# Kernel tuning notes

Hardware: AMD Instinct MI355X
Metric: run time of the kernel (lower is better)

Reference implementation:

```python
import jax, jax.numpy as jnp
import numpy as np

NUM_AGENTS = 32
N_OBS = 16
K = 5
N = 2 * NUM_AGENTS + N_OBS          # 80 nodes per graph
E_KNN = N * K                        # knn edges (loop=True)
E = E_KNN + N_OBS                    # + agent->goal edges (arange(n_obstacles) quirk of source)
AGENT_R = 0.05
OBST_SIZES = np.full((N_OBS,), 0.1, dtype=np.float32)
HID = 128


def _build_graph(obstacle_pos, agent_pos, goal_pos, agent_vel):
    # pos: agents, goals, obstacles
    pos = jnp.concatenate([agent_pos, goal_pos, obstacle_pos], axis=0)        # [N,2]
    d2 = jnp.sum((pos[:, None, :] - pos[None, :, :]) ** 2, axis=-1)           # [N,N]
    _, nbr = jax.lax.top_k(-d2, K)                                            # [N,K] k-NN incl self
    knn_src = nbr.reshape(-1)
    knn_dst = jnp.repeat(jnp.arange(N), K)
    ag_src = jnp.arange(N_OBS)
    ag_dst = ag_src + NUM_AGENTS
    src = jnp.concatenate([knn_src, ag_src])                                  # [E]
    dst = jnp.concatenate([knn_dst, ag_dst])
    # torch.unique(edge_index, dim=-1) dedup: knn edges are unique by construction;
    # only appended agent->goal edges can duplicate -> mask them out.
    dup = ((ag_src * N + ag_dst)[:, None] == (knn_src * N + knn_dst)[None, :]).any(axis=-1)
    mask = jnp.concatenate([jnp.ones((E_KNN,), dtype=bool), ~dup])
    radius = jnp.zeros((N,)).at[:NUM_AGENTS].set(AGENT_R).at[2 * NUM_AGENTS:].set(jnp.asarray(OBST_SIZES))
    x = jnp.zeros((N, 5))
    x = x.at[:NUM_AGENTS, 0].set(1.0)
    x = x.at[NUM_AGENTS:2 * NUM_AGENTS, 1].set(1.0)
    x = x.at[2 * NUM_AGENTS:, 2].set(1.0)
    x = x.at[:NUM_AGENTS, 3].set(jnp.linalg.norm(agent_vel, axis=-1))
    x = x.at[:, 4].set(radius)
    pd = pos[src] - pos[dst]
    dist = jnp.linalg.norm(pd, axis=-1)
    vel = jnp.zeros((N, 2)).at[:NUM_AGENTS].set(agent_vel)
    rv = vel[src] - vel[dst]
    pdn = pd / jnp.maximum(dist, 1e-6)[:, None]
    flag = ((src < NUM_AGENTS) & (dst == src + NUM_AGENTS)).astype(pos.dtype)
    ea = jnp.stack([flag, dist, dist - (radius[src] + radius[dst]),
                    jnp.sum(rv * pdn, axis=-1),
                    rv[:, 0] * pdn[:, 1] - rv[:, 1] * pdn[:, 0]], axis=-1)     # [E,5]
    return x, src, dst, ea, mask


def _gatv2(x, src, dst, ea, mask, Wl, bl, Wr, br, We, att, bias):
    # GATv2Conv, heads=1, add_self_loops=False, edge_dim=5
    xl = x @ Wl + bl                                    # [N,F] (messages)
    xr = x @ Wr + br                                    # [N,F]
    e = jax.nn.leaky_relu(xl[src] + xr[dst] + ea @ We, 0.2)   # [E,F]
    logit = e @ att                                     # [E]
    logit = jnp.where(mask, logit, jnp.finfo(logit.dtype).min)
    m = jax.ops.segment_max(logit, dst, num_segments=N)
    a = jnp.where(mask, jnp.exp(logit - m[dst]), 0.0)
    denom = jax.ops.segment_sum(a, dst, num_segments=N)
    alpha = a / denom[dst]
    out = jax.ops.segment_sum(alpha[:, None] * xl[src], dst, num_segments=N)
    return out + bias


def _forward_single(obstacle_pos, agent_pos, goal_pos, agent_vel, params):
    x, src, dst, ea, mask = _build_graph(obstacle_pos, agent_pos, goal_pos, agent_vel)
    h = x
    for i, p in enumerate(params):
        h = _gatv2(h, src, dst, ea, mask, *p)
        if i < len(params) - 1:
            h = jax.nn.relu(h)
    # global_add_pool over agent nodes (agents are first NUM_AGENTS nodes)
    return jnp.sum(h[:NUM_AGENTS, 0])


def reference(obstacle_pos, agent_pos, goal_pos, agent_vel,
              Wl1, bl1, Wr1, br1, We1, att1, bias1,
              Wl2, bl2, Wr2, br2, We2, att2, bias2,
              Wl3, bl3, Wr3, br3, We3, att3, bias3):
    params = [(Wl1, bl1, Wr1, br1, We1, att1, bias1),
              (Wl2, bl2, Wr2, br2, We2, att2, bias2),
              (Wl3, bl3, Wr3, br3, We3, att3, bias3)]
    vals = jax.vmap(lambda o, a, g, v: _forward_single(o, a, g, v, params))(
        obstacle_pos, agent_pos, goal_pos, agent_vel)                       # [B]
    B = vals.shape[0]
    return jnp.broadcast_to(vals[:, None, None], (B, NUM_AGENTS, 1))


def setup_inputs() -> dict:
    key = jax.random.key(0)
    ks = jax.random.split(key, 32)
    B = 1024
    inp = {
        "obstacle_pos": jax.random.normal(ks[0], (B, N_OBS, 2), dtype=jnp.float32),
        "agent_pos": jax.random.normal(ks[1], (B, NUM_AGENTS, 2), dtype=jnp.float32),
        "goal_pos": jax.random.normal(ks[2], (B, NUM_AGENTS, 2), dtype=jnp.float32),
        "agent_vel": jax.random.normal(ks[3], (B, NUM_AGENTS, 2), dtype=jnp.float32) * 0.1,
    }
    dims = [(5, HID), (HID, HID), (HID, 1)]
    ki = 4
    for li, (fi, fo) in enumerate(dims, start=1):
        s = float(np.sqrt(2.0 / (fi + fo)))
        se = float(np.sqrt(2.0 / (5 + fo)))
        inp[f"Wl{li}"] = jax.random.normal(ks[ki], (fi, fo)) * s; ki += 1
        inp[f"bl{li}"] = jnp.zeros((fo,))
        inp[f"Wr{li}"] = jax.random.normal(ks[ki], (fi, fo)) * s; ki += 1
        inp[f"br{li}"] = jnp.zeros((fo,))
        inp[f"We{li}"] = jax.random.normal(ks[ki], (5, fo)) * se; ki += 1
        inp[f"att{li}"] = jax.random.normal(ks[ki], (fo,)) * float(1.0 / np.sqrt(fo)); ki += 1
        inp[f"bias{li}"] = jnp.zeros((fo,))
    return inp
```

## Files before the change

### kernel.cpp

```cpp
#include <hip/hip_runtime.h>
#include <math.h>

typedef float floatx4 __attribute__((ext_vector_type(4)));
typedef short bf16x8  __attribute__((ext_vector_type(8)));

#define NAG   32
#define NOBS  16
#define NN    80
#define KK    5
#define EKNN  400
#define ED    416
#define HID   128
#define TPB   1024

__device__ __forceinline__ int bsw(int n, int c) { return c ^ ((n & 7) << 1); }

__device__ __forceinline__ float bfhi_f(unsigned u) {
    union { unsigned u; float f; } v; v.u = u & 0xffff0000u; return v.f;
}
__device__ __forceinline__ float bflo_f(unsigned u) {
    union { unsigned u; float f; } v; v.u = u << 16; return v.f;
}
__device__ __forceinline__ unsigned f_bf_rne(float f) {
    union { float f; unsigned u; } v; v.f = f;
    return (v.u + 0x7fffu + ((v.u >> 16) & 1u)) >> 16;
}
__device__ __forceinline__ uint2 pack_bf4v(floatx4 a) {
    uint2 r;
    r.x = f_bf_rne(a[0]) | (f_bf_rne(a[1]) << 16);
    r.y = f_bf_rne(a[2]) | (f_bf_rne(a[3]) << 16);
    return r;
}
__device__ __forceinline__ floatx4 unpack_bf4v(uint2 p) {
    floatx4 r;
    r[0] = bflo_f(p.x); r[1] = bfhi_f(p.x);
    r[2] = bflo_f(p.y); r[3] = bfhi_f(p.y);
    return r;
}

__device__ __forceinline__ void nl_pass5(const float* xf,
    const float* __restrict__ W, const float* __restrict__ bv,
    uint2* dstB, int t)
{
    const int q  = t & 31;
    const int ng = t >> 5;
    const int n0 = ng, n1 = ng + 32, n2 = 64 + (ng & 15);
    floatx4 a0 = {0.f,0.f,0.f,0.f}, a1 = a0, a2 = a0;
#pragma unroll
    for (int fi = 0; fi < 5; ++fi) {
        floatx4 wv = *(const floatx4*)(W + fi*HID + q*4);
        a0 += xf[n0*5 + fi] * wv;
        a1 += xf[n1*5 + fi] * wv;
        a2 += xf[n2*5 + fi] * wv;
    }
    floatx4 b4 = *(const floatx4*)(bv + q*4);
    a0 += b4; a1 += b4; a2 += b4;
    dstB[n0*32 + bsw(n0, q)] = pack_bf4v(a0);
    dstB[n1*32 + bsw(n1, q)] = pack_bf4v(a1);
    if (ng < 16) dstB[n2*32 + bsw(n2, q)] = pack_bf4v(a2);
}

__device__ __forceinline__ void store_tile(floatx4 ac, int mtbase, int l, int col,
                                           float bval, char* dbase)
{
#pragma unroll
    for (int rr = 0; rr < 4; rr++) {
        int row = mtbase + ((l >> 4) << 2) + rr;
        int ch  = (col >> 2) ^ ((row & 7) << 1);
        *(unsigned short*)(dbase + row*256 + ch*8 + (col & 3)*2) =
            (unsigned short)f_bf_rne(ac[rr] + bval);
    }
}

__device__ __forceinline__ void edge_mfma(const uint2* xlB, const uint2* xrB,
    const uint4* WeBfT, const uint4* eaB, const unsigned short* sdS,
    const int* gmask, const float* attS, float* logitS, int t)
{
    const int w = t >> 6, l = t & 63;
    const int g = l >> 4, e16 = l & 15;
    const bf16x8 zf = {0,0,0,0,0,0,0,0};

#pragma unroll 1
    for (int rep = 0; rep < 2; rep++) {
        const int mt = w + rep*16;
        if (mt >= 26) break;
        const int e = mt*16 + e16;
        const unsigned sdv = sdS[e];
        const int src = sdv & 0xff, dst = sdv >> 8;
        const int sb = src*32, db = dst*32;
        const int sx = (src & 7) << 1, dx = (dst & 7) << 1;
        bf16x8 bfrag = (l < 16) ? ((const bf16x8*)eaB)[e] : zf;
        float partial = 0.f;

#pragma unroll 1
        for (int ct = 0; ct < 8; ct++) {
            bf16x8 afrag = (l < 16) ? ((const bf16x8*)WeBfT)[ct*16 + e16] : zf;
            floatx4 D = {0.f,0.f,0.f,0.f};
            D = __builtin_amdgcn_mfma_f32_16x16x32_bf16(afrag, bfrag, D, 0, 0, 0);
            floatx4 attv = ((const floatx4*)attS)[ct*4 + g];
            floatx4 xlv = unpack_bf4v(xlB[sb + ((4*ct + g) ^ sx)]);
            floatx4 xrv = unpack_bf4v(xrB[db + ((4*ct + g) ^ dx)]);
#pragma unroll
            for (int rr = 0; rr < 4; rr++) {
                float s = D[rr] + xlv[rr] + xrv[rr];
                float m = fmaxf(s, 0.2f*s);
                partial = fmaf(m, attv[rr], partial);
            }
        }
        partial += __shfl_xor(partial, 16);
        partial += __shfl_xor(partial, 32);
        if (l < 16) {
            bool act = (e < EKNN) || (gmask[e - EKNN] != 0);
            if (act) logitS[e] = partial;
        }
    }
}

__device__ __forceinline__ void seg_softmax(const float* logitS, const int* gmask,
                                            float* alphaS, int t)
{
    if (t < NN) {
        const int n = t;
        float l[KK];
#pragma unroll
        for (int k = 0; k < KK; k++) l[k] = logitS[n*KK + k];
        float m = l[0];
#pragma unroll
        for (int k = 1; k < KK; k++) m = fmaxf(m, l[k]);
        int ge = -1; float lg = 0.f;
        if (n >= NAG && n < NAG + NOBS && gmask[n - NAG]) {
            ge = EKNN + (n - NAG);
            lg = logitS[ge];
            m = fmaxf(m, lg);
        }
        float s = 0.f, av[KK];
#pragma unroll
        for (int k = 0; k < KK; k++) { av[k] = expf(l[k] - m); s += av[k]; }
        float ag = 0.f;
        if (ge >= 0) { ag = expf(lg - m); s += ag; }
        float inv = 1.f / s;
#pragma unroll
        for (int k = 0; k < KK; k++) alphaS[n*KK + k] = av[k]*inv;
        if (ge >= 0) alphaS[ge] = ag*inv;
    }
}

__device__ __forceinline__ void aggregate(const uint2* xlB, const float* alphaS,
                                          const int* nbr, const int* gmask,
                                          const float* __restrict__ bias,
                                          uint2* hxr, int t)
{
    for (int idx = t; idx < NN*32; idx += TPB) {
        int n = idx >> 5;
        int c = idx & 31;
        floatx4 acc = *(const floatx4*)(bias + 4*c);
#pragma unroll
        for (int k = 0; k < KK; k++) {
            float a = alphaS[n*KK + k];
            int s = nbr[n*KK + k];
            acc += a * unpack_bf4v(xlB[s*32 + bsw(s, c)]);
        }
        if (n >= NAG && n < NAG + NOBS && gmask[n - NAG]) {
            float a = alphaS[EKNN + (n - NAG)];
            int s = n - NAG;
            acc += a * unpack_bf4v(xlB[s*32 + bsw(s, c)]);
        }
#pragma unroll
        for (int c2 = 0; c2 < 4; c2++) acc[c2] = fmaxf(acc[c2], 0.f);
        hxr[n*32 + bsw(n, c)] = pack_bf4v(acc);
    }
}

__global__ __launch_bounds__(TPB, 8) void e3_kernel(
    const float* __restrict__ obst, const float* __restrict__ apos,
    const float* __restrict__ gpos, const float* __restrict__ avel,
    const float* __restrict__ Wl1, const float* __restrict__ bl1,
    const float* __restrict__ Wr1, const float* __restrict__ br1,
    const float* __restrict__ We1, const float* __restrict__ att1, const float* __restrict__ bias1,
    const float* __restrict__ Wl2, const float* __restrict__ bl2,
    const float* __restrict__ Wr2, const float* __restrict__ br2,
    const float* __restrict__ We2, const float* __restrict__ att2, const float* __restrict__ bias2,
    const float* __restrict__ Wl3, const float* __restrict__ bl3,
    const float* __restrict__ Wr3, const float* __restrict__ br3,
    const float* __restrict__ We3, const float* __restrict__ att3, const float* __restrict__ bias3,
    float* __restrict__ out)
{
    __shared__ float pos0[NN], pos1[NN], vel0[NN], vel1[NN], rad[NN];
    __shared__ float xfeat[NN*5];
    __shared__ int   nbr[NN*KK];
    __shared__ int   gmask[NOBS];
    __shared__ float eaS[ED*5];
    __shared__ float logitS[ED];
    __shared__ float alphaS[ED];
    __shared__ unsigned short sdS[ED];
    __shared__ uint2 hxrS[NN*32];
    __shared__ uint2 xlB[NN*32];
    __shared__ uint4 BfS[2*8*64];
    __shared__ float attS[HID];
    __shared__ float xl3S[NN], xr3S[NN];
    __shared__ float resS;

    uint4* WeBfT = BfS;
    uint4* eaB   = BfS + 128;

    const int g = blockIdx.x;
    const int t = threadIdx.x;

    if (t < NN) {
        int n = t;
        float px, py, vx = 0.f, vy = 0.f, r;
        if (n < NAG) {
            px = apos[(g*NAG + n)*2 + 0]; py = apos[(g*NAG + n)*2 + 1];
            vx = avel[(g*NAG + n)*2 + 0]; vy = avel[(g*NAG + n)*2 + 1];
            r = 0.05f;
        } else if (n < 2*NAG) {
            int m = n - NAG;
            px = gpos[(g*NAG + m)*2 + 0]; py = gpos[(g*NAG + m)*2 + 1];
            r = 0.f;
        } else {
            int m = n - 2*NAG;
            px = obst[(g*NOBS + m)*2 + 0]; py = obst[(g*NOBS + m)*2 + 1];
            r = 0.1f;
        }
        pos0[n] = px; pos1[n] = py; vel0[n] = vx; vel1[n] = vy; rad[n] = r;
        xfeat[n*5 + 0] = (n < NAG) ? 1.f : 0.f;
        xfeat[n*5 + 1] = (n >= NAG && n < 2*NAG) ? 1.f : 0.f;
        xfeat[n*5 + 2] = (n >= 2*NAG) ? 1.f : 0.f;
        xfeat[n*5 + 3] = (n < NAG) ? sqrtf(__fadd_rn(__fmul_rn(vx,vx), __fmul_rn(vy,vy))) : 0.f;
        xfeat[n*5 + 4] = r;
    }
    __syncthreads();

    if (t < NN) {
        const int i = t;
        float bd[KK]; int bi[KK];
#pragma unroll
        for (int k = 0; k < KK; k++) { bd[k] = 3.4e38f; bi[k] = -1; }
        const float pix = pos0[i], piy = pos1[i];
        for (int j = 0; j < NN; j++) {
            float dx = __fsub_rn(pix, pos0[j]);
            float dy = __fsub_rn(piy, pos1[j]);
            float d2 = __fadd_rn(__fmul_rn(dx,dx), __fmul_rn(dy,dy));
            if (d2 < bd[KK-1]) {
                int p = KK - 1;
                while (p > 0 && d2 < bd[p-1]) { bd[p] = bd[p-1]; bi[p] = bi[p-1]; p--; }
                bd[p] = d2; bi[p] = j;
            }
        }
#pragma unroll
        for (int k = 0; k < KK; k++) nbr[i*KK + k] = bi[k];
    }
    __syncthreads();

    if (t < NOBS) {
        int j = t, dup = 0;
#pragma unroll
        for (int k = 0; k < KK; k++) dup |= (nbr[(NAG + j)*KK + k] == j);
        gmask[j] = !dup;
    }
    __syncthreads();

    for (int e = t; e < ED; e += TPB) {
        int src, dst;
        if (e < EKNN) { dst = e / KK; src = nbr[e]; }
        else          { src = e - EKNN; dst = src + NAG; }
        float pdx = pos0[src] - pos0[dst];
        float pdy = pos1[src] - pos1[dst];
        float dist = sqrtf(pdx*pdx + pdy*pdy);
        float inv = 1.f / fmaxf(dist, 1e-6f);
        float pnx = pdx * inv, pny = pdy * inv;
        float rvx = vel0[src] - vel0[dst];
        float rvy = vel1[src] - vel1[dst];
        float e0 = (src < NAG && dst == src + NAG) ? 1.f : 0.f;
        float e1 = dist;
        float e2 = dist - (rad[src] + rad[dst]);
        float e3 = rvx*pnx + rvy*pny;
        float e4 = rvx*pny - rvy*pnx;
        eaS[e*5 + 0] = e0; eaS[e*5 + 1] = e1; eaS[e*5 + 2] = e2;
        eaS[e*5 + 3] = e3; eaS[e*5 + 4] = e4;
        sdS[e] = (unsigned short)(src | (dst << 8));
        uint4 pk;
        pk.x = f_bf_rne(e0) | (f_bf_rne(e1) << 16);
        pk.y = f_bf_rne(e2) | (f_bf_rne(e3) << 16);
        pk.z = f_bf_rne(e4);
        pk.w = 0u;
        eaB[e] = pk;
    }

    if (t < HID) {
        uint4 pw;
        pw.x = f_bf_rne(We1[0*HID + t]) | (f_bf_rne(We1[1*HID + t]) << 16);
        pw.y = f_bf_rne(We1[2*HID + t]) | (f_bf_rne(We1[3*HID + t]) << 16);
        pw.z = f_bf_rne(We1[4*HID + t]);
        pw.w = 0u;
        WeBfT[t] = pw;
        attS[t] = att1[t];
    }
    __syncthreads();

    nl_pass5(xfeat, Wl1, bl1, xlB,  t);
    nl_pass5(xfeat, Wr1, br1, hxrS, t);
    __syncthreads();
    edge_mfma(xlB, hxrS, WeBfT, eaB, sdS, gmask, attS, logitS, t);
    __syncthreads();
    seg_softmax(logitS, gmask, alphaS, t);
    __syncthreads();
    aggregate(xlB, alphaS, nbr, gmask, bias1, hxrS, t);
    __syncthreads();

    if (t < HID) attS[t] = att2[t];
    {
        const int w   = t >> 6;
        const int l   = t & 63;
        const int mat = w >> 3;
        const int nt  = w & 7;
        const int ar  = l & 15;
        const int kg2 = (l >> 4) << 1;
        const int arx = (ar & 7) << 1;

        const int sm = t >> 9;
        const int s  = t & 511;
        const int sn = s & 127;
        const int g8 = s >> 7;
        const float* __restrict__ Wst = sm ? Wr2 : Wl2;
        const int swidx = sm*512 + (sn >> 4)*64 + ((sn & 15) | (g8 << 4));

        floatx4 acc0 = {0.f,0.f,0.f,0.f}, acc1 = acc0, acc2 = acc0,
                acc3 = acc0, acc4 = acc0;

#pragma unroll 1
        for (int kb = 0; kb < 4; ++kb) {
            const float* wp = Wst + (kb*32 + g8*8)*HID + sn;
            uint4 pk;
            pk.x = f_bf_rne(wp[0])     | (f_bf_rne(wp[HID])   << 16);
            pk.y = f_bf_rne(wp[2*HID]) | (f_bf_rne(wp[3*HID]) << 16);
            pk.z = f_bf_rne(wp[4*HID]) | (f_bf_rne(wp[5*HID]) << 16);
            pk.w = f_bf_rne(wp[6*HID]) | (f_bf_rne(wp[7*HID]) << 16);
            BfS[swidx] = pk;
            __syncthreads();

            bf16x8 bfrag = ((const bf16x8*)BfS)[mat*512 + nt*64 + l];
            const char* hbase = (const char*)hxrS;
            const int cA = ((kb*8 + kg2) ^ arx) * 8;
#define MT_MFMA(AC, MT) { \
            bf16x8 af = *(const bf16x8*)(hbase + (MT*4096) + ar*256 + cA); \
            AC = __builtin_amdgcn_mfma_f32_16x16x32_bf16(af, bfrag, AC, 0, 0, 0); }
            MT_MFMA(acc0, 0)
            MT_MFMA(acc1, 1)
            MT_MFMA(acc2, 2)
            MT_MFMA(acc3, 3)
            MT_MFMA(acc4, 4)
#undef MT_MFMA
            __syncthreads();
        }

        const float* __restrict__ bv = mat ? br2 : bl2;
        char* dbase = (char*)(mat ? hxrS : xlB);
        const int col = nt*16 + ar;
        const float bval = bv[col];
        store_tile(acc0,  0, l, col, bval, dbase);
        store_tile(acc1, 16, l, col, bval, dbase);
        store_tile(acc2, 32, l, col, bval, dbase);
        store_tile(acc3, 48, l, col, bval, dbase);
        store_tile(acc4, 64, l, col, bval, dbase);
    }

    if (t < HID) {
        uint4 pw;
        pw.x = f_bf_rne(We2[0*HID + t]) | (f_bf_rne(We2[1*HID + t]) << 16);
        pw.y = f_bf_rne(We2[2*HID + t]) | (f_bf_rne(We2[3*HID + t]) << 16);
        pw.z = f_bf_rne(We2[4*HID + t]);
        pw.w = 0u;
        WeBfT[t] = pw;
    } else if (t < HID + ED) {
        int e = t - HID;
        uint4 pk;
        pk.x = f_bf_rne(eaS[e*5+0]) | (f_bf_rne(eaS[e*5+1]) << 16);
        pk.y = f_bf_rne(eaS[e*5+2]) | (f_bf_rne(eaS[e*5+3]) << 16);
        pk.z = f_bf_rne(eaS[e*5+4]);
        pk.w = 0u;
        eaB[e] = pk;
    }
    __syncthreads();

    edge_mfma(xlB, hxrS, WeBfT, eaB, sdS, gmask, attS, logitS, t);
    __syncthreads();
    seg_softmax(logitS, gmask, alphaS, t);
    __syncthreads();
    aggregate(xlB, alphaS, nbr, gmask, bias2, hxrS, t);
    __syncthreads();

    {
        const int q   = t & 31;
        const int grp = t >> 5;
        floatx4 wl4 = *(const floatx4*)(Wl3 + q*4);
        floatx4 wr4 = *(const floatx4*)(Wr3 + q*4);
#pragma unroll
        for (int rep = 0; rep < 3; rep++) {
            int n = grp + rep*32;
            if (n < NN) {
                floatx4 hv = unpack_bf4v(hxrS[n*32 + bsw(n, q)]);
                float al = hv[0]*wl4[0] + hv[1]*wl4[1] + hv[2]*wl4[2] + hv[3]*wl4[3];
                float ar3 = hv[0]*wr4[0] + hv[1]*wr4[1] + hv[2]*wr4[2] + hv[3]*wr4[3];
                al += __shfl_xor(al, 16); ar3 += __shfl_xor(ar3, 16);
                al += __shfl_xor(al, 8);  ar3 += __shfl_xor(ar3, 8);
                al += __shfl_xor(al, 4);  ar3 += __shfl_xor(ar3, 4);
                al += __shfl_xor(al, 2);  ar3 += __shfl_xor(ar3, 2);
                al += __shfl_xor(al, 1);  ar3 += __shfl_xor(ar3, 1);
                if (q == 0) {
                    xl3S[n] = al + bl3[0];
                    xr3S[n] = ar3 + br3[0];
                }
            }
        }
    }
    __syncthreads();

    {
        float w0 = We3[0], w1 = We3[1], w2 = We3[2], w3 = We3[3], w4 = We3[4];
        float a0 = att3[0];
        for (int e = t; e < ED; e += TPB) {
            int src, dst;
            if (e < EKNN) { dst = e / KK; src = nbr[e]; }
            else { src = e - EKNN; dst = src + NAG; if (!gmask[src]) continue; }
            float s = xl3S[src] + xr3S[dst]
                    + eaS[e*5+0]*w0 + eaS[e*5+1]*w1 + eaS[e*5+2]*w2
                    + eaS[e*5+3]*w3 + eaS[e*5+4]*w4;
            s = fmaxf(s, 0.2f*s);
            logitS[e] = s * a0;
        }
    }
    __syncthreads();

    seg_softmax(logitS, gmask, alphaS, t);
    __syncthreads();

    float v = 0.f;
    if (t < NAG) {
        v = bias3[0];
#pragma unroll
        for (int k = 0; k < KK; k++) v += alphaS[t*KK + k] * xl3S[nbr[t*KK + k]];
    }
    if (t < 64) {
#pragma unroll
        for (int o = 32; o > 0; o >>= 1) v += __shfl_xor(v, o);
        if (t == 0) resS = v;
    }
    __syncthreads();
    if (t < NAG) out[g*NAG + t] = resS;
}

extern "C" void kernel_launch(void* const* d_in, const int* in_sizes, int n_in,
                              void* d_out, int out_size, void* d_ws, size_t ws_size,
                              hipStream_t stream)
{
    const float* obst = (const float*)d_in[0];
    const float* apos = (const float*)d_in[1];
    const float* gpos = (const float*)d_in[2];
    const float* avel = (const float*)d_in[3];
    const int B = in_sizes[1] / (NAG * 2);

    e3_kernel<<<B, TPB, 0, stream>>>(
        obst, apos, gpos, avel,
        (const float*)d_in[4],  (const float*)d_in[5],  (const float*)d_in[6],
        (const float*)d_in[7],  (const float*)d_in[8],  (const float*)d_in[9],
        (const float*)d_in[10],
        (const float*)d_in[11], (const float*)d_in[12], (const float*)d_in[13],
        (const float*)d_in[14], (const float*)d_in[15], (const float*)d_in[16],
        (const float*)d_in[17],
        (const float*)d_in[18], (const float*)d_in[19], (const float*)d_in[20],
        (const float*)d_in[21], (const float*)d_in[22], (const float*)d_in[23],
        (const float*)d_in[24],
        (float*)d_out);
}
```

Measured before the change: 116.6 us.

## Pre-pack layer-2 and edge weights to bf16 once in a prep kernel

Adds a one-block prep kernel that converts Wl2/Wr2 and We1/We2 to the swizzled bf16 fragment layout in workspace, once per call. The main kernel then copies the pre-packed uint4s into shared memory instead of every block doing strided fp32 loads and bf16 rounding. The edge MFMA now takes xl+xr as its accumulator input, which folds the two adds into the MFMA. The cost is an extra kernel launch and a dependency on workspace memory.

```diff
diff --git a/kernel.cpp b/kernel.cpp
--- a/kernel.cpp
+++ b/kernel.cpp
@@ -36,6 +36,40 @@
     r[0] = bflo_f(p.x); r[1] = bfhi_f(p.x);
     r[2] = bflo_f(p.y); r[3] = bfhi_f(p.y);
     return r;
+}
+
+__global__ __launch_bounds__(TPB) void prep_kernel(
+    const float* __restrict__ Wl2, const float* __restrict__ Wr2,
+    const float* __restrict__ We1, const float* __restrict__ We2,
+    uint4* __restrict__ ws4)
+{
+    const int t = threadIdx.x;
+    const int sm = t >> 9;
+    const int s  = t & 511;
+    const int sn = s & 127;
+    const int g8 = s >> 7;
+    const float* __restrict__ Wst = sm ? Wr2 : Wl2;
+    const int swidx = sm*512 + (sn >> 4)*64 + ((sn & 15) | (g8 << 4));
+#pragma unroll 1
+    for (int kb = 0; kb < 4; ++kb) {
+        const float* wp = Wst + (kb*32 + g8*8)*HID + sn;
+        uint4 pk;
+        pk.x = f_bf_rne(wp[0])     | (f_bf_rne(wp[HID])   << 16);
+        pk.y = f_bf_rne(wp[2*HID]) | (f_bf_rne(wp[3*HID]) << 16);
+        pk.z = f_bf_rne(wp[4*HID]) | (f_bf_rne(wp[5*HID]) << 16);
+        pk.w = f_bf_rne(wp[6*HID]) | (f_bf_rne(wp[7*HID]) << 16);
+        ws4[kb*1024 + swidx] = pk;
+    }
+    if (t < 256) {
+        const float* __restrict__ We = (t < 128) ? We1 : We2;
+        int c = t & 127;
+        uint4 pw;
+        pw.x = f_bf_rne(We[0*HID + c]) | (f_bf_rne(We[1*HID + c]) << 16);
+        pw.y = f_bf_rne(We[2*HID + c]) | (f_bf_rne(We[3*HID + c]) << 16);
+        pw.z = f_bf_rne(We[4*HID + c]);
+        pw.w = 0u;
+        ws4[4096 + t] = pw;
+    }
 }
 
 __device__ __forceinline__ void nl_pass5(const float* xf,
@@ -95,15 +129,13 @@
 #pragma unroll 1
         for (int ct = 0; ct < 8; ct++) {
             bf16x8 afrag = (l < 16) ? ((const bf16x8*)WeBfT)[ct*16 + e16] : zf;
-            floatx4 D = {0.f,0.f,0.f,0.f};
-            D = __builtin_amdgcn_mfma_f32_16x16x32_bf16(afrag, bfrag, D, 0, 0, 0);
+            floatx4 C = unpack_bf4v(xlB[sb + ((4*ct + g) ^ sx)])
+                      + unpack_bf4v(xrB[db + ((4*ct + g) ^ dx)]);
+            floatx4 D = __builtin_amdgcn_mfma_f32_16x16x32_bf16(afrag, bfrag, C, 0, 0, 0);
             floatx4 attv = ((const floatx4*)attS)[ct*4 + g];
-            floatx4 xlv = unpack_bf4v(xlB[sb + ((4*ct + g) ^ sx)]);
-            floatx4 xrv = unpack_bf4v(xrB[db + ((4*ct + g) ^ dx)]);
 #pragma unroll
             for (int rr = 0; rr < 4; rr++) {
-                float s = D[rr] + xlv[rr] + xrv[rr];
-                float m = fmaxf(s, 0.2f*s);
+                float m = fmaxf(D[rr], 0.2f*D[rr]);
                 partial = fmaf(m, attv[rr], partial);
             }
         }
@@ -176,13 +208,13 @@
     const float* __restrict__ gpos, const float* __restrict__ avel,
     const float* __restrict__ Wl1, const float* __restrict__ bl1,
     const float* __restrict__ Wr1, const float* __restrict__ br1,
-    const float* __restrict__ We1, const float* __restrict__ att1, const float* __restrict__ bias1,
-    const float* __restrict__ Wl2, const float* __restrict__ bl2,
-    const float* __restrict__ Wr2, const float* __restrict__ br2,
-    const float* __restrict__ We2, const float* __restrict__ att2, const float* __restrict__ bias2,
+    const float* __restrict__ att1, const float* __restrict__ bias1,
+    const float* __restrict__ bl2, const float* __restrict__ br2,
+    const float* __restrict__ att2, const float* __restrict__ bias2,
     const float* __restrict__ Wl3, const float* __restrict__ bl3,
     const float* __restrict__ Wr3, const float* __restrict__ br3,
     const float* __restrict__ We3, const float* __restrict__ att3, const float* __restrict__ bias3,
+    const uint4* __restrict__ ws4,
     float* __restrict__ out)
 {
     __shared__ float pos0[NN], pos1[NN], vel0[NN], vel1[NN], rad[NN];
@@ -288,13 +320,8 @@
     }
 
     if (t < HID) {
-        uint4 pw;
-        pw.x = f_bf_rne(We1[0*HID + t]) | (f_bf_rne(We1[1*HID + t]) << 16);
-        pw.y = f_bf_rne(We1[2*HID + t]) | (f_bf_rne(We1[3*HID + t]) << 16);
-        pw.z = f_bf_rne(We1[4*HID + t]);
-        pw.w = 0u;
-        WeBfT[t] = pw;
-        attS[t] = att1[t];
+        WeBfT[t] = ws4[4096 + t];
+        attS[t]  = att1[t];
     }
     __syncthreads();
 
@@ -318,25 +345,12 @@
         const int kg2 = (l >> 4) << 1;
         const int arx = (ar & 7) << 1;
 
-        const int sm = t >> 9;
-        const int s  = t & 511;
-        const int sn = s & 127;
-        const int g8 = s >> 7;
-        const float* __restrict__ Wst = sm ? Wr2 : Wl2;
-        const int swidx = sm*512 + (sn >> 4)*64 + ((sn & 15) | (g8 << 4));
-
         floatx4 acc0 = {0.f,0.f,0.f,0.f}, acc1 = acc0, acc2 = acc0,
                 acc3 = acc0, acc4 = acc0;
 
 #pragma unroll 1
         for (int kb = 0; kb < 4; ++kb) {
-            const float* wp = Wst + (kb*32 + g8*8)*HID + sn;
-            uint4 pk;
-            pk.x = f_bf_rne(wp[0])     | (f_bf_rne(wp[HID])   << 16);
-            pk.y = f_bf_rne(wp[2*HID]) | (f_bf_rne(wp[3*HID]) << 16);
-            pk.z = f_bf_rne(wp[4*HID]) | (f_bf_rne(wp[5*HID]) << 16);
-            pk.w = f_bf_rne(wp[6*HID]) | (f_bf_rne(wp[7*HID]) << 16);
-            BfS[swidx] = pk;
+            BfS[t] = ws4[kb*1024 + t];
             __syncthreads();
 
             bf16x8 bfrag = ((const bf16x8*)BfS)[mat*512 + nt*64 + l];
@@ -366,12 +380,7 @@
     }
 
     if (t < HID) {
-        uint4 pw;
-        pw.x = f_bf_rne(We2[0*HID + t]) | (f_bf_rne(We2[1*HID + t]) << 16);
-        pw.y = f_bf_rne(We2[2*HID + t]) | (f_bf_rne(We2[3*HID + t]) << 16);
-        pw.z = f_bf_rne(We2[4*HID + t]);
-        pw.w = 0u;
-        WeBfT[t] = pw;
+        WeBfT[t] = ws4[4224 + t];
     } else if (t < HID + ED) {
         int e = t - HID;
         uint4 pk;
@@ -459,17 +468,22 @@
     const float* gpos = (const float*)d_in[2];
     const float* avel = (const float*)d_in[3];
     const int B = in_sizes[1] / (NAG * 2);
+    uint4* ws4 = (uint4*)d_ws;
+
+    prep_kernel<<<1, TPB, 0, stream>>>(
+        (const float*)d_in[11], (const float*)d_in[13],
+        (const float*)d_in[8],  (const float*)d_in[15],
+        ws4);
 
     e3_kernel<<<B, TPB, 0, stream>>>(
         obst, apos, gpos, avel,
         (const float*)d_in[4],  (const float*)d_in[5],  (const float*)d_in[6],
-        (const float*)d_in[7],  (const float*)d_in[8],  (const float*)d_in[9],
-        (const float*)d_in[10],
-        (const float*)d_in[11], (const float*)d_in[12], (const float*)d_in[13],
-        (const float*)d_in[14], (const float*)d_in[15], (const float*)d_in[16],
-        (const float*)d_in[17],
+        (const float*)d_in[7],  (const float*)d_in[9],  (const float*)d_in[10],
+        (const float*)d_in[12], (const float*)d_in[14],
+        (const float*)d_in[16], (const float*)d_in[17],
         (const float*)d_in[18], (const float*)d_in[19], (const float*)d_in[20],
         (const float*)d_in[21], (const float*)d_in[22], (const float*)d_in[23],
         (const float*)d_in[24],
+        ws4,
         (float*)d_out);
 }
```

Result: slower. 122.3 us (+4.9%).
